# Kernel tuning notes

Measured on AMD Instinct MI355X. Metric: run time of the kernel, lower is better.

The kernel has to match this reference:

```python
import jax, jax.numpy as jnp
import numpy as np

B, P, D, H = 2048, 128, 64, 8
DB = 10  # D_obs + D_pos = 7 + 3, hard-coded in the module


def setup_inputs() -> dict:
    key = jax.random.key(0)
    ks = jax.random.split(key, 10)
    s = lambda fan_in: 1.0 / np.sqrt(fan_in)
    return {
        "x": jax.random.normal(ks[0], (B, D), dtype=jnp.float32),
        "b": jax.random.normal(ks[1], (B, P, DB), dtype=jnp.float32),
        "W_kvx": jax.random.uniform(ks[2], (D, 2 * H * D), jnp.float32, -s(D), s(D)),
        "b_kvx": jax.random.uniform(ks[3], (2 * H * D,), jnp.float32, -s(D), s(D)),
        "W_kvb": jax.random.uniform(ks[4], (DB, 2 * H * D), jnp.float32, -s(DB), s(DB)),
        "b_kvb": jax.random.uniform(ks[5], (2 * H * D,), jnp.float32, -s(DB), s(DB)),
        "W_q": jax.random.uniform(ks[6], (D, H * D), jnp.float32, -s(D), s(D)),
        "b_q": jax.random.uniform(ks[7], (H * D,), jnp.float32, -s(D), s(D)),
        "W_f": jax.random.uniform(ks[8], (H * D, D), jnp.float32, -s(H * D), s(H * D)),
        "b_f": jax.random.uniform(ks[9], (D,), jnp.float32, -s(H * D), s(H * D)),
    }


def reference(x, b, W_kvx, b_kvx, W_kvb, b_kvb, W_q, b_q, W_f, b_f):
    Bn, Dx = x.shape
    _, Pn, _ = b.shape
    # dual projections + broadcast add: [B,1,2HD] + [B,P,2HD]
    kv = (x @ W_kvx + b_kvx)[:, None, :] + (jnp.einsum('bpe,ef->bpf', b, W_kvb) + b_kvb)
    k, v = jnp.split(kv, 2, axis=-1)            # each [B,P,H*D]
    k = k.reshape(Bn, Pn, H, Dx)
    v = v.reshape(Bn, Pn, H, Dx)
    q = (x @ W_q + b_q).reshape(Bn, H, Dx)
    dots = jnp.einsum('bphd,bhd->bph', k, q) / np.sqrt(Dx).astype(np.float32)
    # NOTE: faithful to source — softmax over the HEAD axis (last dim of [B,P,H])
    attn = jax.nn.softmax(dots, axis=-1)
    vals = jnp.einsum('bph,bphd->bhd', attn, v)  # sum over positions P
    out = vals.reshape(Bn, H * Dx) @ W_f + b_f
    return out
```

## Files before the change

kernel.cpp:

```cpp
#include <hip/hip_runtime.h>

#define NDB 10

__global__ __launch_bounds__(256) void fused_attn(
    const float* __restrict__ x, const float* __restrict__ bmat,
    const float* __restrict__ W_kvx, const float* __restrict__ b_kvx,
    const float* __restrict__ W_kvb, const float* __restrict__ b_kvb,
    const float* __restrict__ W_q, const float* __restrict__ b_q,
    const float* __restrict__ W_f, const float* __restrict__ b_f,
    float* __restrict__ out)
{
    __shared__ float x_t[64][4];
    __shared__ float bb_s[4][1280];
    __shared__ float xp_s[4][1024];
    __shared__ float q_s[4][512];
    __shared__ float dot0_s[4][8];
    __shared__ float Wqkb_s[4][NDB][8];
    __shared__ float A_s[4][8];
    __shared__ float S_s[4][NDB][8];
    __shared__ float vals_s[512][4];
    __shared__ float pout[4][4][64];

    const int t = threadIdx.x;
    const int b0 = blockIdx.x * 4;
    const int lane = t & 63;
    const int w = t >> 6;

    x_t[t & 63][t >> 6] = x[b0 * 64 + t];
    {
        const float4* src = (const float4*)(bmat + (size_t)b0 * 1280);
        float4* dst = (float4*)bb_s;
        #pragma unroll
        for (int it = 0; it < 5; ++it) dst[t + 256 * it] = src[t + 256 * it];
    }
    __syncthreads();

    {
        float accKV[4][4] = {};
        float accQ[4][2] = {};
        const float* pkv = W_kvx + t;
        const float* pq  = W_q  + t;
        #pragma unroll 4
        for (int k = 0; k < 64; ++k) {
            float4 xv = *(const float4*)&x_t[k][0];
            float xr[4] = {xv.x, xv.y, xv.z, xv.w};
            float wkv[4], wq[2];
            #pragma unroll
            for (int c = 0; c < 4; ++c) wkv[c] = pkv[k * 1024 + c * 256];
            #pragma unroll
            for (int c = 0; c < 2; ++c) wq[c] = pq[k * 512 + c * 256];
            #pragma unroll
            for (int r = 0; r < 4; ++r) {
                #pragma unroll
                for (int c = 0; c < 4; ++c) accKV[r][c] = fmaf(xr[r], wkv[c], accKV[r][c]);
                #pragma unroll
                for (int c = 0; c < 2; ++c) accQ[r][c]  = fmaf(xr[r], wq[c],  accQ[r][c]);
            }
        }
        #pragma unroll
        for (int c = 0; c < 4; ++c) {
            int f = c * 256 + t;
            float bias = b_kvx[f] + b_kvb[f];
            #pragma unroll
            for (int rr = 0; rr < 4; ++rr) xp_s[rr][f] = accKV[rr][c] + bias;
        }
        #pragma unroll
        for (int c = 0; c < 2; ++c) {
            int fq = c * 256 + t;
            float bias = b_q[fq];
            #pragma unroll
            for (int rr = 0; rr < 4; ++rr) q_s[rr][fq] = accQ[rr][c] + bias;
        }
    }
    __syncthreads();

    const int r = w;

    {
        int h = lane >> 3, i8 = lane & 7;
        float s = 0.f;
        #pragma unroll
        for (int j = 0; j < 8; ++j) {
            int d = h * 64 + i8 + j * 8;
            s = fmaf(xp_s[r][d], q_s[r][d], s);
        }
        s += __shfl_xor(s, 1); s += __shfl_xor(s, 2); s += __shfl_xor(s, 4);
        if (i8 == 0) dot0_s[r][h] = s;
    }
    {
        int g = lane >> 3, l = lane & 7;
        #pragma unroll
        for (int e = 0; e < NDB; ++e) {
            float s = 0.f;
            #pragma unroll
            for (int m = 0; m < 8; ++m) {
                int d = g * 64 + l + m * 8;
                s = fmaf(W_kvb[e * 1024 + d], q_s[r][d], s);
            }
            s += __shfl_xor(s, 1); s += __shfl_xor(s, 2); s += __shfl_xor(s, 4);
            if (l == 0) Wqkb_s[r][e][g] = s;
        }
    }
    __syncthreads();

    {
        int h = lane & 7, pg = lane >> 3;
        float aA = 0.f, aS[NDB];
        #pragma unroll
        for (int e = 0; e < NDB; ++e) aS[e] = 0.f;
        #pragma unroll 4
        for (int it = 0; it < 16; ++it) {
            int p = pg + 8 * it;
            float dot = dot0_s[r][h];
            #pragma unroll
            for (int e = 0; e < NDB; ++e)
                dot = fmaf(bb_s[r][p * NDB + e], Wqkb_s[r][e][h], dot);
            dot *= 0.125f;
            float m = dot;
            m = fmaxf(m, __shfl_xor(m, 1));
            m = fmaxf(m, __shfl_xor(m, 2));
            m = fmaxf(m, __shfl_xor(m, 4));
            float ex = __expf(dot - m);
            float sum = ex;
            sum += __shfl_xor(sum, 1); sum += __shfl_xor(sum, 2); sum += __shfl_xor(sum, 4);
            float at = ex * __builtin_amdgcn_rcpf(sum);
            aA += at;
            #pragma unroll
            for (int e = 0; e < NDB; ++e) aS[e] = fmaf(at, bb_s[r][p * NDB + e], aS[e]);
        }
        aA += __shfl_xor(aA, 8); aA += __shfl_xor(aA, 16); aA += __shfl_xor(aA, 32);
        #pragma unroll
        for (int e = 0; e < NDB; ++e) {
            aS[e] += __shfl_xor(aS[e], 8);
            aS[e] += __shfl_xor(aS[e], 16);
            aS[e] += __shfl_xor(aS[e], 32);
        }
        if (pg == 0) {
            A_s[r][h] = aA;
            #pragma unroll
            for (int e = 0; e < NDB; ++e) S_s[r][e][h] = aS[e];
        }
    }
    __syncthreads();

    #pragma unroll
    for (int i = 0; i < 8; ++i) {
        int f = lane + 64 * i;
        float v = A_s[r][i] * xp_s[r][512 + f];
        #pragma unroll
        for (int e = 0; e < NDB; ++e)
            v = fmaf(S_s[r][e][i], W_kvb[e * 1024 + 512 + f], v);
        vals_s[f][r] = v;
    }
    __syncthreads();

    {
        const int j = t & 63, fs = t >> 6;
        float acc0 = 0.f, acc1 = 0.f, acc2 = 0.f, acc3 = 0.f;
        #pragma unroll 4
        for (int fi = 0; fi < 128; ++fi) {
            int f = fs * 128 + fi;
            float4 v = *(const float4*)&vals_s[f][0];
            float wf = W_f[f * 64 + j];
            acc0 = fmaf(v.x, wf, acc0);
            acc1 = fmaf(v.y, wf, acc1);
            acc2 = fmaf(v.z, wf, acc2);
            acc3 = fmaf(v.w, wf, acc3);
        }
        pout[fs][0][j] = acc0; pout[fs][1][j] = acc1;
        pout[fs][2][j] = acc2; pout[fs][3][j] = acc3;
    }
    __syncthreads();
    {
        const int rr = t >> 6, j = t & 63;
        float o = pout[0][rr][j] + pout[1][rr][j] + pout[2][rr][j] + pout[3][rr][j] + b_f[j];
        out[(size_t)(b0 + rr) * 64 + j] = o;
    }
}

extern "C" void kernel_launch(void* const* d_in, const int* in_sizes, int n_in,
                              void* d_out, int out_size, void* d_ws, size_t ws_size,
                              hipStream_t stream)
{
    const float* x     = (const float*)d_in[0];
    const float* bmat  = (const float*)d_in[1];
    const float* W_kvx = (const float*)d_in[2];
    const float* b_kvx = (const float*)d_in[3];
    const float* W_kvb = (const float*)d_in[4];
    const float* b_kvb = (const float*)d_in[5];
    const float* W_q   = (const float*)d_in[6];
    const float* b_q   = (const float*)d_in[7];
    const float* W_f   = (const float*)d_in[8];
    const float* b_f   = (const float*)d_in[9];
    float* out = (float*)d_out;

    fused_attn<<<512, 256, 0, stream>>>(x, bmat, W_kvx, b_kvx, W_kvb, b_kvb,
                                        W_q, b_q, W_f, b_f, out);
}
```

Baseline: 105.5 us.

## Prefetch bmat into registers across the projection GEMM and drop wave-local barriers

The per-row bmat tile is now loaded into registers at kernel start and written to shared memory only after the x projection GEMM. This lets the global load latency overlap with the FMA loop instead of stalling at the first barrier. Two __syncthreads are removed where each wave only reads shared data it wrote itself. The x_t and vals_s layouts are transposed to row-major so the GEMMs can use float4 loads along k, and the bmat values are hoisted into registers for reuse in the softmax loop. The cost is higher register pressure from holding five float4s through the GEMM, which may reduce occupancy. Dropping the barriers relies on intra-wave ordering of LDS accesses.

```diff
diff --git a/kernel.cpp b/kernel.cpp
--- a/kernel.cpp
+++ b/kernel.cpp
@@ -10,7 +10,7 @@
     const float* __restrict__ W_f, const float* __restrict__ b_f,
     float* __restrict__ out)
 {
-    __shared__ float x_t[64][4];
+    __shared__ float x_t[4][64];
     __shared__ float bb_s[4][1280];
     __shared__ float xp_s[4][1024];
     __shared__ float q_s[4][512];
@@ -18,7 +18,7 @@
     __shared__ float Wqkb_s[4][NDB][8];
     __shared__ float A_s[4][8];
     __shared__ float S_s[4][NDB][8];
-    __shared__ float vals_s[512][4];
+    __shared__ float vals_s[4][512];
     __shared__ float pout[4][4][64];
 
     const int t = threadIdx.x;
@@ -26,51 +26,64 @@
     const int lane = t & 63;
     const int w = t >> 6;
 
-    x_t[t & 63][t >> 6] = x[b0 * 64 + t];
-    {
-        const float4* src = (const float4*)(bmat + (size_t)b0 * 1280);
-        float4* dst = (float4*)bb_s;
-        #pragma unroll
-        for (int it = 0; it < 5; ++it) dst[t + 256 * it] = src[t + 256 * it];
-    }
-    __syncthreads();
-
-    {
-        float accKV[4][4] = {};
-        float accQ[4][2] = {};
+    float xval = x[b0 * 64 + t];
+    float4 bbreg[5];
+    const float4* bsrc = (const float4*)(bmat + (size_t)b0 * 1280);
+    #pragma unroll
+    for (int it = 0; it < 5; ++it) bbreg[it] = bsrc[t + 256 * it];
+    x_t[t >> 6][t & 63] = xval;
+    __syncthreads();
+
+    float accKV[4][4] = {};
+    float accQ[4][2] = {};
+    {
         const float* pkv = W_kvx + t;
-        const float* pq  = W_q  + t;
+        const float* pq  = W_q + t;
         #pragma unroll 4
-        for (int k = 0; k < 64; ++k) {
-            float4 xv = *(const float4*)&x_t[k][0];
-            float xr[4] = {xv.x, xv.y, xv.z, xv.w};
-            float wkv[4], wq[2];
-            #pragma unroll
-            for (int c = 0; c < 4; ++c) wkv[c] = pkv[k * 1024 + c * 256];
-            #pragma unroll
-            for (int c = 0; c < 2; ++c) wq[c] = pq[k * 512 + c * 256];
-            #pragma unroll
-            for (int r = 0; r < 4; ++r) {
+        for (int k0 = 0; k0 < 64; k0 += 4) {
+            float4 xr[4];
+            #pragma unroll
+            for (int r = 0; r < 4; ++r) xr[r] = *(const float4*)&x_t[r][k0];
+            #pragma unroll
+            for (int kk = 0; kk < 4; ++kk) {
+                const int k = k0 + kk;
+                float wk0 = pkv[k * 1024];
+                float wk1 = pkv[k * 1024 + 256];
+                float wk2 = pkv[k * 1024 + 512];
+                float wk3 = pkv[k * 1024 + 768];
+                float wq0 = pq[k * 512];
+                float wq1 = pq[k * 512 + 256];
                 #pragma unroll
-                for (int c = 0; c < 4; ++c) accKV[r][c] = fmaf(xr[r], wkv[c], accKV[r][c]);
-                #pragma unroll
-                for (int c = 0; c < 2; ++c) accQ[r][c]  = fmaf(xr[r], wq[c],  accQ[r][c]);
+                for (int r = 0; r < 4; ++r) {
+                    float xv = ((const float*)&xr[r])[kk];
+                    accKV[r][0] = fmaf(xv, wk0, accKV[r][0]);
+                    accKV[r][1] = fmaf(xv, wk1, accKV[r][1]);
+                    accKV[r][2] = fmaf(xv, wk2, accKV[r][2]);
+                    accKV[r][3] = fmaf(xv, wk3, accKV[r][3]);
+                    accQ[r][0]  = fmaf(xv, wq0, accQ[r][0]);
+                    accQ[r][1]  = fmaf(xv, wq1, accQ[r][1]);
+                }
             }
         }
+    }
+    {
         #pragma unroll
         for (int c = 0; c < 4; ++c) {
             int f = c * 256 + t;
             float bias = b_kvx[f] + b_kvb[f];
             #pragma unroll
-            for (int rr = 0; rr < 4; ++rr) xp_s[rr][f] = accKV[rr][c] + bias;
+            for (int r = 0; r < 4; ++r) xp_s[r][f] = accKV[r][c] + bias;
         }
         #pragma unroll
         for (int c = 0; c < 2; ++c) {
             int fq = c * 256 + t;
             float bias = b_q[fq];
             #pragma unroll
-            for (int rr = 0; rr < 4; ++rr) q_s[rr][fq] = accQ[rr][c] + bias;
-        }
+            for (int r = 0; r < 4; ++r) q_s[r][fq] = accQ[r][c] + bias;
+        }
+        float4* bbdst = (float4*)bb_s;
+        #pragma unroll
+        for (int it = 0; it < 5; ++it) bbdst[t + 256 * it] = bbreg[it];
     }
     __syncthreads();
 
@@ -101,7 +114,6 @@
             if (l == 0) Wqkb_s[r][e][g] = s;
         }
     }
-    __syncthreads();
 
     {
         int h = lane & 7, pg = lane >> 3;
@@ -111,10 +123,12 @@
         #pragma unroll 4
         for (int it = 0; it < 16; ++it) {
             int p = pg + 8 * it;
+            float bbv[NDB];
+            #pragma unroll
+            for (int e = 0; e < NDB; ++e) bbv[e] = bb_s[r][p * NDB + e];
             float dot = dot0_s[r][h];
             #pragma unroll
-            for (int e = 0; e < NDB; ++e)
-                dot = fmaf(bb_s[r][p * NDB + e], Wqkb_s[r][e][h], dot);
+            for (int e = 0; e < NDB; ++e) dot = fmaf(bbv[e], Wqkb_s[r][e][h], dot);
             dot *= 0.125f;
             float m = dot;
             m = fmaxf(m, __shfl_xor(m, 1));
@@ -126,7 +140,7 @@
             float at = ex * __builtin_amdgcn_rcpf(sum);
             aA += at;
             #pragma unroll
-            for (int e = 0; e < NDB; ++e) aS[e] = fmaf(at, bb_s[r][p * NDB + e], aS[e]);
+            for (int e = 0; e < NDB; ++e) aS[e] = fmaf(at, bbv[e], aS[e]);
         }
         aA += __shfl_xor(aA, 8); aA += __shfl_xor(aA, 16); aA += __shfl_xor(aA, 32);
         #pragma unroll
@@ -141,7 +155,6 @@
             for (int e = 0; e < NDB; ++e) S_s[r][e][h] = aS[e];
         }
     }
-    __syncthreads();
 
     #pragma unroll
     for (int i = 0; i < 8; ++i) {
@@ -150,30 +163,37 @@
         #pragma unroll
         for (int e = 0; e < NDB; ++e)
             v = fmaf(S_s[r][e][i], W_kvb[e * 1024 + 512 + f], v);
-        vals_s[f][r] = v;
+        vals_s[r][f] = v;
     }
     __syncthreads();
 
     {
         const int j = t & 63, fs = t >> 6;
-        float acc0 = 0.f, acc1 = 0.f, acc2 = 0.f, acc3 = 0.f;
+        float acc[4] = {};
         #pragma unroll 4
-        for (int fi = 0; fi < 128; ++fi) {
-            int f = fs * 128 + fi;
-            float4 v = *(const float4*)&vals_s[f][0];
-            float wf = W_f[f * 64 + j];
-            acc0 = fmaf(v.x, wf, acc0);
-            acc1 = fmaf(v.y, wf, acc1);
-            acc2 = fmaf(v.z, wf, acc2);
-            acc3 = fmaf(v.w, wf, acc3);
-        }
-        pout[fs][0][j] = acc0; pout[fs][1][j] = acc1;
-        pout[fs][2][j] = acc2; pout[fs][3][j] = acc3;
+        for (int f0 = fs * 128; f0 < fs * 128 + 128; f0 += 4) {
+            float w0 = W_f[(f0 + 0) * 64 + j];
+            float w1 = W_f[(f0 + 1) * 64 + j];
+            float w2 = W_f[(f0 + 2) * 64 + j];
+            float w3 = W_f[(f0 + 3) * 64 + j];
+            #pragma unroll
+            for (int rr = 0; rr < 4; ++rr) {
+                float4 v = *(const float4*)&vals_s[rr][f0];
+                acc[rr] = fmaf(v.x, w0, acc[rr]);
+                acc[rr] = fmaf(v.y, w1, acc[rr]);
+                acc[rr] = fmaf(v.z, w2, acc[rr]);
+                acc[rr] = fmaf(v.w, w3, acc[rr]);
+            }
+        }
+        #pragma unroll
+        for (int rr = 0; rr < 4; ++rr) pout[fs][rr][j] = acc[rr];
     }
     __syncthreads();
     {
         const int rr = t >> 6, j = t & 63;
-        float o = pout[0][rr][j] + pout[1][rr][j] + pout[2][rr][j] + pout[3][rr][j] + b_f[j];
+        float o = b_f[j];
+        #pragma unroll
+        for (int fs = 0; fs < 4; ++fs) o += pout[fs][rr][j];
         out[(size_t)(b0 + rr) * 64 + j] = o;
     }
 }
```

After: 124.2 us. +17.8%, slower.

## Split fused attention into tiled projection, per-row attention, and output GEMM kernels

Applied to the files above, without the earlier changes.

Splits the single fused kernel into three launches. The first is a 64-row tiled register-blocked GEMM for the x projections (KV and Q), writing to a workspace. The second computes per-row attention with one wave per row and no block-wide barriers. The third is an output GEMM that stages W_f tiles in shared memory. The aim is better reuse of the projection weights than the old 4-rows-per-block layout, which reread W_kvx/W_q from global for every 4 rows. The cost is extra workspace traffic (about 12 MB of XQ plus 4 MB of VALS written and read back) and two more launches.

```diff
diff --git a/kernel.cpp b/kernel.cpp
--- a/kernel.cpp
+++ b/kernel.cpp
@@ -2,119 +2,150 @@
 
 #define NDB 10
 
-__global__ __launch_bounds__(256) void fused_attn(
-    const float* __restrict__ x, const float* __restrict__ bmat,
-    const float* __restrict__ W_kvx, const float* __restrict__ b_kvx,
-    const float* __restrict__ W_kvb, const float* __restrict__ b_kvb,
+__global__ __launch_bounds__(256) void proj_kernel(
+    const float* __restrict__ x, const float* __restrict__ W_kvx,
+    const float* __restrict__ b_kvx, const float* __restrict__ b_kvb,
     const float* __restrict__ W_q, const float* __restrict__ b_q,
-    const float* __restrict__ W_f, const float* __restrict__ b_f,
-    float* __restrict__ out)
-{
-    __shared__ float x_t[64][4];
-    __shared__ float bb_s[4][1280];
-    __shared__ float xp_s[4][1024];
-    __shared__ float q_s[4][512];
+    float* __restrict__ XQ)
+{
+    __shared__ float x_t[64][68];
+    const int t = threadIdx.x;
+    const int row0 = blockIdx.x * 64;
+    const int ct = blockIdx.y;
+
+    {
+        const int r = t & 63, kb = (t >> 6) * 16;
+        float4 xv[4];
+        #pragma unroll
+        for (int i = 0; i < 4; ++i)
+            xv[i] = *(const float4*)&x[(size_t)(row0 + r) * 64 + kb + i * 4];
+        #pragma unroll
+        for (int i = 0; i < 4; ++i) {
+            x_t[kb + i * 4 + 0][r] = xv[i].x;
+            x_t[kb + i * 4 + 1][r] = xv[i].y;
+            x_t[kb + i * 4 + 2][r] = xv[i].z;
+            x_t[kb + i * 4 + 3][r] = xv[i].w;
+        }
+    }
+    __syncthreads();
+
+    const bool iskv = (ct < 16);
+    const int c0 = (iskv ? ct * 64 : (ct - 16) * 64) + (t & 15) * 4;
+    const int stride = iskv ? 1024 : 512;
+    const float* Wp = (iskv ? W_kvx : W_q) + c0;
+    const int r0 = (t >> 4) * 4;
+
+    float acc[4][4] = {};
+    #pragma unroll 8
+    for (int k = 0; k < 64; ++k) {
+        float4 a  = *(const float4*)&x_t[k][r0];
+        float4 wv = *(const float4*)&Wp[k * stride];
+        float av[4] = {a.x, a.y, a.z, a.w};
+        float wvv[4] = {wv.x, wv.y, wv.z, wv.w};
+        #pragma unroll
+        for (int i = 0; i < 4; ++i)
+            #pragma unroll
+            for (int jj = 0; jj < 4; ++jj)
+                acc[i][jj] = fmaf(av[i], wvv[jj], acc[i][jj]);
+    }
+    float4 bias;
+    if (iskv) {
+        float4 b1 = *(const float4*)&b_kvx[c0];
+        float4 b2 = *(const float4*)&b_kvb[c0];
+        bias.x = b1.x + b2.x; bias.y = b1.y + b2.y;
+        bias.z = b1.z + b2.z; bias.w = b1.w + b2.w;
+    } else {
+        bias = *(const float4*)&b_q[c0];
+    }
+    const int outcol = ct * 64 + (t & 15) * 4;
+    #pragma unroll
+    for (int i = 0; i < 4; ++i) {
+        float4 o;
+        o.x = acc[i][0] + bias.x; o.y = acc[i][1] + bias.y;
+        o.z = acc[i][2] + bias.z; o.w = acc[i][3] + bias.w;
+        *(float4*)&XQ[(size_t)(row0 + r0 + i) * 1536 + outcol] = o;
+    }
+}
+
+__global__ __launch_bounds__(256) void attn_core(
+    const float* __restrict__ bmat, const float* __restrict__ W_kvb,
+    const float* __restrict__ XQ, float* __restrict__ VALS)
+{
+    __shared__ float bb_s[4][128][11];
+    __shared__ float q_s[4][8][68];
     __shared__ float dot0_s[4][8];
     __shared__ float Wqkb_s[4][NDB][8];
     __shared__ float A_s[4][8];
     __shared__ float S_s[4][NDB][8];
-    __shared__ float vals_s[512][4];
-    __shared__ float pout[4][4][64];
-
-    const int t = threadIdx.x;
-    const int b0 = blockIdx.x * 4;
-    const int lane = t & 63;
-    const int w = t >> 6;
-
-    x_t[t & 63][t >> 6] = x[b0 * 64 + t];
-    {
-        const float4* src = (const float4*)(bmat + (size_t)b0 * 1280);
-        float4* dst = (float4*)bb_s;
-        #pragma unroll
-        for (int it = 0; it < 5; ++it) dst[t + 256 * it] = src[t + 256 * it];
-    }
-    __syncthreads();
-
-    {
-        float accKV[4][4] = {};
-        float accQ[4][2] = {};
-        const float* pkv = W_kvx + t;
-        const float* pq  = W_q  + t;
-        #pragma unroll 4
-        for (int k = 0; k < 64; ++k) {
-            float4 xv = *(const float4*)&x_t[k][0];
-            float xr[4] = {xv.x, xv.y, xv.z, xv.w};
-            float wkv[4], wq[2];
-            #pragma unroll
-            for (int c = 0; c < 4; ++c) wkv[c] = pkv[k * 1024 + c * 256];
-            #pragma unroll
-            for (int c = 0; c < 2; ++c) wq[c] = pq[k * 512 + c * 256];
-            #pragma unroll
-            for (int r = 0; r < 4; ++r) {
-                #pragma unroll
-                for (int c = 0; c < 4; ++c) accKV[r][c] = fmaf(xr[r], wkv[c], accKV[r][c]);
-                #pragma unroll
-                for (int c = 0; c < 2; ++c) accQ[r][c]  = fmaf(xr[r], wq[c],  accQ[r][c]);
-            }
-        }
+
+    const int t = threadIdx.x, lane = t & 63, w = t >> 6;
+    const int row = blockIdx.x * 4 + w;
+    const float* __restrict__ xq = XQ + (size_t)row * 1536;
+
+    {
+        float4 a  = *(const float4*)&xq[1024 + lane * 4];
+        float4 b4 = *(const float4*)&xq[1024 + 256 + lane * 4];
+        int d0 = lane * 4;
+        float av[4] = {a.x, a.y, a.z, a.w};
+        float bv[4] = {b4.x, b4.y, b4.z, b4.w};
         #pragma unroll
         for (int c = 0; c < 4; ++c) {
-            int f = c * 256 + t;
-            float bias = b_kvx[f] + b_kvb[f];
-            #pragma unroll
-            for (int rr = 0; rr < 4; ++rr) xp_s[rr][f] = accKV[rr][c] + bias;
-        }
-        #pragma unroll
-        for (int c = 0; c < 2; ++c) {
-            int fq = c * 256 + t;
-            float bias = b_q[fq];
-            #pragma unroll
-            for (int rr = 0; rr < 4; ++rr) q_s[rr][fq] = accQ[rr][c] + bias;
-        }
-    }
-    __syncthreads();
-
-    const int r = w;
-
-    {
-        int h = lane >> 3, i8 = lane & 7;
+            int d = d0 + c;
+            q_s[w][d >> 6][d & 63] = av[c];
+            int d2 = d + 256;
+            q_s[w][d2 >> 6][d2 & 63] = bv[c];
+        }
+    }
+    {
+        const float* bsrc = bmat + (size_t)row * 1280;
+        #pragma unroll
+        for (int i = 0; i < 20; ++i) {
+            int idx = lane + 64 * i;
+            bb_s[w][idx / 10][idx % 10] = bsrc[idx];
+        }
+    }
+
+    const int h = lane >> 3, i8 = lane & 7;
+    {
         float s = 0.f;
         #pragma unroll
         for (int j = 0; j < 8; ++j) {
-            int d = h * 64 + i8 + j * 8;
-            s = fmaf(xp_s[r][d], q_s[r][d], s);
+            int d = i8 + 8 * j;
+            s = fmaf(xq[h * 64 + d], q_s[w][h][d], s);
         }
         s += __shfl_xor(s, 1); s += __shfl_xor(s, 2); s += __shfl_xor(s, 4);
-        if (i8 == 0) dot0_s[r][h] = s;
-    }
-    {
-        int g = lane >> 3, l = lane & 7;
-        #pragma unroll
-        for (int e = 0; e < NDB; ++e) {
-            float s = 0.f;
-            #pragma unroll
-            for (int m = 0; m < 8; ++m) {
-                int d = g * 64 + l + m * 8;
-                s = fmaf(W_kvb[e * 1024 + d], q_s[r][d], s);
-            }
-            s += __shfl_xor(s, 1); s += __shfl_xor(s, 2); s += __shfl_xor(s, 4);
-            if (l == 0) Wqkb_s[r][e][g] = s;
-        }
-    }
-    __syncthreads();
-
-    {
-        int h = lane & 7, pg = lane >> 3;
+        if (i8 == 0) dot0_s[w][h] = s;
+    }
+    #pragma unroll
+    for (int e = 0; e < NDB; ++e) {
+        float s = 0.f;
+        #pragma unroll
+        for (int m = 0; m < 8; ++m) {
+            int d = i8 + 8 * m;
+            s = fmaf(W_kvb[e * 1024 + h * 64 + d], q_s[w][h][d], s);
+        }
+        s += __shfl_xor(s, 1); s += __shfl_xor(s, 2); s += __shfl_xor(s, 4);
+        if (i8 == 0) Wqkb_s[w][e][h] = s;
+    }
+
+    {
+        const int hh = lane & 7, pg = lane >> 3;
         float aA = 0.f, aS[NDB];
         #pragma unroll
         for (int e = 0; e < NDB; ++e) aS[e] = 0.f;
+        float wq[NDB];
+        #pragma unroll
+        for (int e = 0; e < NDB; ++e) wq[e] = Wqkb_s[w][e][hh];
+        const float d0v = dot0_s[w][hh];
         #pragma unroll 4
         for (int it = 0; it < 16; ++it) {
             int p = pg + 8 * it;
-            float dot = dot0_s[r][h];
-            #pragma unroll
-            for (int e = 0; e < NDB; ++e)
-                dot = fmaf(bb_s[r][p * NDB + e], Wqkb_s[r][e][h], dot);
+            float bbv[NDB];
+            #pragma unroll
+            for (int e = 0; e < NDB; ++e) bbv[e] = bb_s[w][p][e];
+            float dot = d0v;
+            #pragma unroll
+            for (int e = 0; e < NDB; ++e) dot = fmaf(bbv[e], wq[e], dot);
             dot *= 0.125f;
             float m = dot;
             m = fmaxf(m, __shfl_xor(m, 1));
@@ -126,7 +157,7 @@
             float at = ex * __builtin_amdgcn_rcpf(sum);
             aA += at;
             #pragma unroll
-            for (int e = 0; e < NDB; ++e) aS[e] = fmaf(at, bb_s[r][p * NDB + e], aS[e]);
+            for (int e = 0; e < NDB; ++e) aS[e] = fmaf(at, bbv[e], aS[e]);
         }
         aA += __shfl_xor(aA, 8); aA += __shfl_xor(aA, 16); aA += __shfl_xor(aA, 32);
         #pragma unroll
@@ -136,46 +167,54 @@
             aS[e] += __shfl_xor(aS[e], 32);
         }
         if (pg == 0) {
-            A_s[r][h] = aA;
-            #pragma unroll
-            for (int e = 0; e < NDB; ++e) S_s[r][e][h] = aS[e];
-        }
-    }
-    __syncthreads();
+            A_s[w][hh] = aA;
+            #pragma unroll
+            for (int e = 0; e < NDB; ++e) S_s[w][e][hh] = aS[e];
+        }
+    }
 
     #pragma unroll
     for (int i = 0; i < 8; ++i) {
         int f = lane + 64 * i;
-        float v = A_s[r][i] * xp_s[r][512 + f];
+        float v = A_s[w][i] * xq[512 + f];
         #pragma unroll
         for (int e = 0; e < NDB; ++e)
-            v = fmaf(S_s[r][e][i], W_kvb[e * 1024 + 512 + f], v);
-        vals_s[f][r] = v;
-    }
-    __syncthreads();
-
-    {
-        const int j = t & 63, fs = t >> 6;
-        float acc0 = 0.f, acc1 = 0.f, acc2 = 0.f, acc3 = 0.f;
-        #pragma unroll 4
-        for (int fi = 0; fi < 128; ++fi) {
-            int f = fs * 128 + fi;
-            float4 v = *(const float4*)&vals_s[f][0];
-            float wf = W_f[f * 64 + j];
-            acc0 = fmaf(v.x, wf, acc0);
-            acc1 = fmaf(v.y, wf, acc1);
-            acc2 = fmaf(v.z, wf, acc2);
-            acc3 = fmaf(v.w, wf, acc3);
-        }
-        pout[fs][0][j] = acc0; pout[fs][1][j] = acc1;
-        pout[fs][2][j] = acc2; pout[fs][3][j] = acc3;
-    }
-    __syncthreads();
-    {
-        const int rr = t >> 6, j = t & 63;
-        float o = pout[0][rr][j] + pout[1][rr][j] + pout[2][rr][j] + pout[3][rr][j] + b_f[j];
-        out[(size_t)(b0 + rr) * 64 + j] = o;
-    }
+            v = fmaf(S_s[w][e][i], W_kvb[e * 1024 + 512 + f], v);
+        VALS[(size_t)row * 512 + f] = v;
+    }
+}
+
+__global__ __launch_bounds__(256) void out_kernel(
+    const float* __restrict__ VALS, const float* __restrict__ W_f,
+    const float* __restrict__ b_f, float* __restrict__ out)
+{
+    __shared__ float wf_s[128][64];
+    const int t = threadIdx.x, j = t & 63;
+    const int row = blockIdx.x * 4 + (t >> 6);
+    const int rowU = __builtin_amdgcn_readfirstlane(row);
+    const float4* vrow = (const float4*)(VALS + (size_t)rowU * 512);
+
+    float acc = 0.f;
+    #pragma unroll
+    for (int kt = 0; kt < 4; ++kt) {
+        __syncthreads();
+        #pragma unroll
+        for (int i = 0; i < 8; ++i) {
+            int fi = t + 256 * i;
+            ((float4*)wf_s)[fi] = ((const float4*)(W_f + kt * 128 * 64))[fi];
+        }
+        __syncthreads();
+        #pragma unroll 8
+        for (int k4 = 0; k4 < 32; ++k4) {
+            float4 v = vrow[kt * 32 + k4];
+            int k = k4 * 4;
+            acc = fmaf(v.x, wf_s[k + 0][j], acc);
+            acc = fmaf(v.y, wf_s[k + 1][j], acc);
+            acc = fmaf(v.z, wf_s[k + 2][j], acc);
+            acc = fmaf(v.w, wf_s[k + 3][j], acc);
+        }
+    }
+    out[(size_t)row * 64 + j] = acc + b_f[j];
 }
 
 extern "C" void kernel_launch(void* const* d_in, const int* in_sizes, int n_in,
@@ -192,8 +231,11 @@
     const float* b_q   = (const float*)d_in[7];
     const float* W_f   = (const float*)d_in[8];
     const float* b_f   = (const float*)d_in[9];
-    float* out = (float*)d_out;
-
-    fused_attn<<<512, 256, 0, stream>>>(x, bmat, W_kvx, b_kvx, W_kvb, b_kvb,
-                                        W_q, b_q, W_f, b_f, out);
-}
+    float* out  = (float*)d_out;
+    float* XQ   = (float*)d_ws;
+    float* VALS = XQ + (size_t)2048 * 1536;
+
+    proj_kernel<<<dim3(32, 24), 256, 0, stream>>>(x, W_kvx, b_kvx, b_kvb, W_q, b_q, XQ);
+    attn_core<<<512, 256, 0, stream>>>(bmat, W_kvb, XQ, VALS);
+    out_kernel<<<512, 256, 0, stream>>>(VALS, W_f, b_f, out);
+}
```

New measurement: 131.6 us. +24.8%, slower.
